# Kernel optimization log

Hardware: AMD Instinct MI355X
Metric: run time of the kernel (lower is better)

## Reference

```python
import jax, jax.numpy as jnp
import numpy as np

B, S, I, H, O = 2048, 128, 1, 512, 1
OUT_SEQ_LEN = 24


def setup_inputs() -> dict:
    key = jax.random.key(0)
    ks = jax.random.split(key, 12)
    s = 1.0 / np.sqrt(H)
    u = lambda k, shape: jax.random.uniform(k, shape, jnp.float32, -s, s)
    return {
        'x': jax.random.normal(ks[0], (B, S, I), jnp.float32),
        'enc_Wih': u(ks[1], (H, I)),
        'enc_Whh': u(ks[2], (H, H)),
        'enc_bih': u(ks[3], (H,)),
        'enc_bhh': u(ks[4], (H,)),
        'dec_Wih': u(ks[5], (H, I)),
        'dec_Whh': u(ks[6], (H, H)),
        'dec_bih': u(ks[7], (H,)),
        'dec_bhh': u(ks[8], (H,)),
        'fc_W': u(ks[9], (O, H)),
        'fc_b': u(ks[10], (O,)),
    }


def reference(x, enc_Wih, enc_Whh, enc_bih, enc_bhh,
              dec_Wih, dec_Whh, dec_bih, dec_bhh, fc_W, fc_b):
    batch = x.shape[0]
    h0 = jnp.zeros((batch, H), x.dtype)

    # Encoder: vanilla tanh RNN, h_t = tanh(x_t W_ih^T + b_ih + h_{t-1} W_hh^T + b_hh)
    def enc_step(h, xt):
        h2 = jnp.tanh(xt @ enc_Wih.T + enc_bih + h @ enc_Whh.T + enc_bhh)
        return h2, None

    hT, _ = jax.lax.scan(enc_step, h0, jnp.swapaxes(x, 0, 1))  # scan over S

    def dec_step(carry, _):
        h, inp = carry
        h2 = jnp.tanh(inp @ dec_Wih.T + dec_bih + h @ dec_Whh.T + dec_bhh)
        out = h2 @ fc_W.T + fc_b  # [B, O]
        return (h2, out), out

    dec_in0 = x[:, -1, :]  # [B, I]
    _, outs = jax.lax.scan(dec_step, (hT, dec_in0), None, length=OUT_SEQ_LEN)
    outputs = jnp.swapaxes(outs, 0, 1)  # [B, OUT_SEQ_LEN, O]
    return outputs[..., 0]  # squeeze(-1) since O == 1
```

## Files before the change

kernel.cpp:

```cpp
#include <hip/hip_runtime.h>
#include <math.h>

#define BATCH 2048
#define SEQ   128
#define HID   512
#define OUTT  24
#define RPB   16
#define NBLK  (BATCH/RPB)
#define TPB   1024
#define NTW   2
#define KTN   (HID/32)
#define LDSB_KT 4
#define STR_KT  (KTN - LDSB_KT)
#define LDSB_BASE 0
#define STR_BASE  LDSB_KT
#define ATILE 8192
#define PFD 4

typedef _Float16 half8 __attribute__((ext_vector_type(8)));
typedef float   floatx4 __attribute__((ext_vector_type(4)));

__device__ __forceinline__ void mfma_hv(floatx4& c, half8 a, half8 b) {
    c = __builtin_amdgcn_mfma_f32_16x16x32_f16(a, b, c, 0, 0, 0);
}

__device__ __forceinline__ float ftanh(float x) {
    float e = __builtin_amdgcn_exp2f(x * 2.885390081777927f);
    float r = __builtin_amdgcn_rcpf(e + 1.0f);
    return fmaf(-2.0f, r, 1.0f);
}

__global__ __launch_bounds__(256) void pack_wfrag(const float* __restrict__ W,
                                                  _Float16* __restrict__ Bw)
{
    int id   = blockIdx.x * 256 + threadIdx.x;
    int lane = id & 63;
    int nt   = (id >> 6) & 31;
    int kt   = id >> 11;
    int n  = nt * 16 + (lane & 15);
    int k0 = kt * 32 + (lane >> 4) * 8;
    const float* src = W + (size_t)n * HID + k0;
    half8 v;
    #pragma unroll
    for (int j = 0; j < 8; j++) v[j] = (_Float16)src[j];
    *(half8*)&Bw[(size_t)id * 8] = v;
}

__global__ __launch_bounds__(TPB)
__attribute__((amdgpu_waves_per_eu(4, 4)))
void rnn_persist(
    const float* __restrict__ x,
    const _Float16* __restrict__ BwE,
    const _Float16* __restrict__ BwD,
    const float* __restrict__ encWih, const float* __restrict__ encBih,
    const float* __restrict__ encBhh,
    const float* __restrict__ decWih, const float* __restrict__ decBih,
    const float* __restrict__ decBhh,
    const float* __restrict__ fcW, const float* __restrict__ fcB,
    float* __restrict__ out)
{
    __shared__ _Float16 A[ATILE];
    __shared__ _Float16 BwL[LDSB_KT * 16384];
    __shared__ float    xs[RPB][SEQ];
    __shared__ float    dec_in_s[RPB];

    const int tid  = threadIdx.x;
    const int lane = tid & 63;
    const int wv   = tid >> 6;
    const int row0 = blockIdx.x * RPB;
    const int c    = lane & 15;
    const int q    = lane >> 4;
    const int mB   = q * 4;

    const float fcb0 = fcB[0];

    int   nIdx[NTW];
    int   moff[NTW][4];
    float wiR[NTW], bbR[NTW];
    #pragma unroll
    for (int i = 0; i < NTW; i++) {
        int n = (wv * NTW + i) * 16 + c;
        nIdx[i] = n;
        int G = (n >> 3) & 3;
        int base = (n >> 5) * 512 + G * 128 + (n & 7);
        #pragma unroll
        for (int r = 0; r < 4; r++)
            moff[i][r] = base + (((mB + r) ^ G) << 3);
        wiR[i] = encWih[n];
        bbR[i] = encBih[n] + encBhh[n];
    }
    int   aFC[HID / 64];
    float fcw[HID / 64];
    #pragma unroll
    for (int ii = 0; ii < HID / 64; ii++) {
        int k = ii * 64 + lane;
        int G = (k >> 3) & 3;
        aFC[ii] = (k >> 5) * 512 + G * 128 + (k & 7) + ((wv ^ G) << 3);
        fcw[ii] = fcW[k];
    }

    {
        const float4* xg = (const float4*)(x + (size_t)row0 * SEQ);
        if (tid < RPB * SEQ / 4) ((float4*)xs)[tid] = xg[tid];
    }

    for (int i = tid; i < ATILE / 2; i += TPB) ((int*)A)[i] = 0;

    {
        const float4* src = (const float4*)(BwE + (size_t)LDSB_BASE * 16384);
        float4* dst = (float4*)BwL;
        #pragma unroll
        for (int i = 0; i < LDSB_KT * 16384 / 8 / TPB; i++)
            dst[i * TPB + tid] = src[i * TPB + tid];
    }

    const int    ldsAoff = q * 128 + ((c ^ q) << 3);
    const size_t bbase   = (size_t)(wv * NTW) * 512 + (size_t)lane * 8;
    const int    bbL     = wv * NTW * 512 + lane * 8;

    __syncthreads();

    for (int t = 0; t < SEQ + OUTT; t++) {
        const bool enc = (t < SEQ);
        const _Float16* __restrict__ Bw = enc ? BwE : BwD;

        if (t == SEQ) {
            #pragma unroll
            for (int i = 0; i < NTW; i++) {
                wiR[i] = decWih[nIdx[i]];
                bbR[i] = decBih[nIdx[i]] + decBhh[nIdx[i]];
            }
            const float4* src = (const float4*)(BwD + (size_t)LDSB_BASE * 16384);
            float4* dst = (float4*)BwL;
            #pragma unroll
            for (int i = 0; i < LDSB_KT * 16384 / 8 / TPB; i++)
                dst[i * TPB + tid] = src[i * TPB + tid];
            __syncthreads();
        }

        floatx4 acc[NTW];
        #pragma unroll
        for (int i = 0; i < NTW; i++) acc[i] = (floatx4){0.f, 0.f, 0.f, 0.f};

        half8 sb[STR_KT][NTW];
        #pragma unroll
        for (int p = 0; p < PFD; p++)
            #pragma unroll
            for (int i = 0; i < NTW; i++)
                sb[p][i] = *(const half8*)&Bw[bbase + (size_t)(STR_BASE + p) * 16384 + i * 512];

        __builtin_amdgcn_s_setprio(1);

        #pragma unroll
        for (int kl = 0; kl < LDSB_KT; kl++) {
            half8 a = *(const half8*)&A[(LDSB_BASE + kl) * 512 + ldsAoff];
            #pragma unroll
            for (int i = 0; i < NTW; i++) {
                half8 b = *(const half8*)&BwL[kl * 16384 + bbL + i * 512];
                mfma_hv(acc[i], a, b);
            }
        }

        #pragma unroll
        for (int s = 0; s < STR_KT; s++) {
            const int kt = STR_BASE + s;
            if (s + PFD < STR_KT) {
                #pragma unroll
                for (int i = 0; i < NTW; i++)
                    sb[s + PFD][i] = *(const half8*)&Bw[bbase + (size_t)(kt + PFD) * 16384 + i * 512];
            }
            half8 a = *(const half8*)&A[kt * 512 + ldsAoff];
            #pragma unroll
            for (int i = 0; i < NTW; i++)
                mfma_hv(acc[i], a, sb[s][i]);
        }

        __builtin_amdgcn_s_setprio(0);

        __syncthreads();

        float inp[4];
        if (enc) {
            #pragma unroll
            for (int r = 0; r < 4; r++) inp[r] = xs[mB + r][t];
        } else if (t == SEQ) {
            #pragma unroll
            for (int r = 0; r < 4; r++) inp[r] = xs[mB + r][SEQ - 1];
        } else {
            #pragma unroll
            for (int r = 0; r < 4; r++) inp[r] = dec_in_s[mB + r];
        }

        #pragma unroll
        for (int i = 0; i < NTW; i++) {
            #pragma unroll
            for (int r = 0; r < 4; r++) {
                float v = ftanh(acc[i][r] + inp[r] * wiR[i] + bbR[i]);
                A[moff[i][r]] = (_Float16)v;
            }
        }
        __syncthreads();

        if (!enc) {
            float sfc = 0.f;
            #pragma unroll
            for (int ii = 0; ii < HID / 64; ii++)
                sfc = fmaf((float)A[aFC[ii]], fcw[ii], sfc);
            #pragma unroll
            for (int off = 32; off > 0; off >>= 1)
                sfc += __shfl_down(sfc, off, 64);
            if (lane == 0) {
                float o = sfc + fcb0;
                dec_in_s[wv] = o;
                out[(size_t)(row0 + wv) * OUTT + (t - SEQ)] = o;
            }
            __syncthreads();
        }
    }
}

extern "C" void kernel_launch(void* const* d_in, const int* in_sizes, int n_in,
                              void* d_out, int out_size, void* d_ws, size_t ws_size,
                              hipStream_t stream)
{
    const float* x        = (const float*)d_in[0];
    const float* enc_Wih  = (const float*)d_in[1];
    const float* enc_Whh  = (const float*)d_in[2];
    const float* enc_bih  = (const float*)d_in[3];
    const float* enc_bhh  = (const float*)d_in[4];
    const float* dec_Wih  = (const float*)d_in[5];
    const float* dec_Whh  = (const float*)d_in[6];
    const float* dec_bih  = (const float*)d_in[7];
    const float* dec_bhh  = (const float*)d_in[8];
    const float* fc_W     = (const float*)d_in[9];
    const float* fc_b     = (const float*)d_in[10];
    float* out = (float*)d_out;

    const size_t wfrag = (size_t)HID * HID;
    _Float16* BwE = (_Float16*)d_ws;
    _Float16* BwD = BwE + wfrag;

    pack_wfrag<<<HID * HID / (256 * 8), 256, 0, stream>>>(enc_Whh, BwE);
    pack_wfrag<<<HID * HID / (256 * 8), 256, 0, stream>>>(dec_Whh, BwD);

    rnn_persist<<<NBLK, TPB, 0, stream>>>(
        x, BwE, BwD,
        enc_Wih, enc_bih, enc_bhh,
        dec_Wih, dec_bih, dec_bhh,
        fc_W, fc_b, out);
}
```

Before: 623.2 us.

## Double-buffer hidden state in LDS and prefetch next-step weights across barrier

```diff
diff --git a/kernel.cpp b/kernel.cpp
--- a/kernel.cpp
+++ b/kernel.cpp
@@ -10,12 +10,13 @@
 #define TPB   1024
 #define NTW   2
 #define KTN   (HID/32)
-#define LDSB_KT 4
+#define LDSB_KT 3
 #define STR_KT  (KTN - LDSB_KT)
 #define LDSB_BASE 0
 #define STR_BASE  LDSB_KT
 #define ATILE 8192
-#define PFD 4
+#define PFD   4
+#define PRIME 2
 
 typedef _Float16 half8 __attribute__((ext_vector_type(8)));
 typedef float   floatx4 __attribute__((ext_vector_type(4)));
@@ -59,7 +60,7 @@
     const float* __restrict__ fcW, const float* __restrict__ fcB,
     float* __restrict__ out)
 {
-    __shared__ _Float16 A[ATILE];
+    __shared__ _Float16 A[2][ATILE];
     __shared__ _Float16 BwL[LDSB_KT * 16384];
     __shared__ float    xs[RPB][SEQ];
     __shared__ float    dec_in_s[RPB];
@@ -104,7 +105,7 @@
         if (tid < RPB * SEQ / 4) ((float4*)xs)[tid] = xg[tid];
     }
 
-    for (int i = tid; i < ATILE / 2; i += TPB) ((int*)A)[i] = 0;
+    for (int i = tid; i < ATILE / 2; i += TPB) ((int*)A[0])[i] = 0;
 
     {
         const float4* src = (const float4*)(BwE + (size_t)LDSB_BASE * 16384);
@@ -118,8 +119,16 @@
     const size_t bbase   = (size_t)(wv * NTW) * 512 + (size_t)lane * 8;
     const int    bbL     = wv * NTW * 512 + lane * 8;
 
+    half8 sb[STR_KT][NTW];
+    #pragma unroll
+    for (int p = 0; p < PRIME; p++)
+        #pragma unroll
+        for (int i = 0; i < NTW; i++)
+            sb[p][i] = *(const half8*)&BwE[bbase + (size_t)(STR_BASE + p) * 16384 + i * 512];
+
     __syncthreads();
 
+    int cur = 0;
     for (int t = 0; t < SEQ + OUTT; t++) {
         const bool enc = (t < SEQ);
         const _Float16* __restrict__ Bw = enc ? BwE : BwD;
@@ -142,18 +151,17 @@
         #pragma unroll
         for (int i = 0; i < NTW; i++) acc[i] = (floatx4){0.f, 0.f, 0.f, 0.f};
 
-        half8 sb[STR_KT][NTW];
-        #pragma unroll
-        for (int p = 0; p < PFD; p++)
+        __builtin_amdgcn_s_setprio(1);
+
+        #pragma unroll
+        for (int p = PRIME; p < PFD; p++)
             #pragma unroll
             for (int i = 0; i < NTW; i++)
                 sb[p][i] = *(const half8*)&Bw[bbase + (size_t)(STR_BASE + p) * 16384 + i * 512];
 
-        __builtin_amdgcn_s_setprio(1);
-
         #pragma unroll
         for (int kl = 0; kl < LDSB_KT; kl++) {
-            half8 a = *(const half8*)&A[(LDSB_BASE + kl) * 512 + ldsAoff];
+            half8 a = *(const half8*)&A[cur][(LDSB_BASE + kl) * 512 + ldsAoff];
             #pragma unroll
             for (int i = 0; i < NTW; i++) {
                 half8 b = *(const half8*)&BwL[kl * 16384 + bbL + i * 512];
@@ -169,7 +177,7 @@
                 for (int i = 0; i < NTW; i++)
                     sb[s + PFD][i] = *(const half8*)&Bw[bbase + (size_t)(kt + PFD) * 16384 + i * 512];
             }
-            half8 a = *(const half8*)&A[kt * 512 + ldsAoff];
+            half8 a = *(const half8*)&A[cur][kt * 512 + ldsAoff];
             #pragma unroll
             for (int i = 0; i < NTW; i++)
                 mfma_hv(acc[i], a, sb[s][i]);
@@ -177,7 +185,16 @@
 
         __builtin_amdgcn_s_setprio(0);
 
-        __syncthreads();
+        const int nxt = cur ^ 1;
+
+        {
+            const _Float16* __restrict__ Bwn = (t + 1 < SEQ) ? BwE : BwD;
+            #pragma unroll
+            for (int p = 0; p < PRIME; p++)
+                #pragma unroll
+                for (int i = 0; i < NTW; i++)
+                    sb[p][i] = *(const half8*)&Bwn[bbase + (size_t)(STR_BASE + p) * 16384 + i * 512];
+        }
 
         float inp[4];
         if (enc) {
@@ -196,16 +213,17 @@
             #pragma unroll
             for (int r = 0; r < 4; r++) {
                 float v = ftanh(acc[i][r] + inp[r] * wiR[i] + bbR[i]);
-                A[moff[i][r]] = (_Float16)v;
+                A[nxt][moff[i][r]] = (_Float16)v;
             }
         }
         __syncthreads();
 
         if (!enc) {
+            const _Float16* An = A[nxt];
             float sfc = 0.f;
             #pragma unroll
             for (int ii = 0; ii < HID / 64; ii++)
-                sfc = fmaf((float)A[aFC[ii]], fcw[ii], sfc);
+                sfc = fmaf((float)An[aFC[ii]], fcw[ii], sfc);
             #pragma unroll
             for (int off = 32; off > 0; off >>= 1)
                 sfc += __shfl_down(sfc, off, 64);
@@ -216,6 +234,7 @@
             }
             __syncthreads();
         }
+        cur = nxt;
     }
 }
 
```

Result: faster. 596.6 us (-4.3%).
